# Kernel optimization log

Measured on AMD Instinct MI355X. Metric: run time of the kernel, lower is better.

Reference implementation:

```python
import jax, jax.numpy as jnp
import numpy as np

# Model dims (match init_kwargs)
D_OUT = 64      # d_in == d_out
SEQ_L = 4096    # input_len
K_EIG = 24      # num_eigh
K_U = 3         # auto_reg_k_u
K_Y = 2         # auto_reg_k_y
BATCH = 8


def get_top_hankel_eigh(n, k):
    """Top-k eigenpairs of the Hankel matrix Z[i,j] = 2/((i+j)^3-(i+j)), 1-indexed."""
    idx = np.arange(1, n + 1, dtype=np.float64)
    s = idx[:, None] + idx[None, :]
    z = 2.0 / (s ** 3 - s)
    vals, vecs = np.linalg.eigh(z)  # ascending
    return (jnp.asarray(vals[-k:], jnp.float32),        # [k]
            jnp.asarray(vecs[:, -k:], jnp.float32))     # [n, k]


def setup_inputs() -> dict:
    key = jax.random.key(0)
    k1, k2, k3, k4 = jax.random.split(key, 4)
    eig_vals, eig_vecs = get_top_hankel_eigh(SEQ_L, K_EIG)
    m_x_var = 1.0 / float(D_OUT) ** 0.5
    return {
        "inputs": jax.random.normal(k1, (BATCH, SEQ_L, D_OUT), jnp.float32),
        "m_y": jax.random.normal(k2, (D_OUT, K_Y, D_OUT), jnp.float32) * 0.01,
        "m_u": jax.random.normal(k3, (D_OUT, D_OUT, K_U), jnp.float32) * m_x_var,
        "m_phi": jax.random.normal(k4, (D_OUT * K_EIG, D_OUT), jnp.float32) * 0.01,
        "eig_vals": eig_vals,
        "eig_vecs": eig_vecs,
    }


def _stu_single(x, m_y, m_u, m_phi, eig_vals, eig_vecs):
    """apply_stu for one sequence x: [L, d] -> [L, d]."""
    L, d = x.shape
    n = 2 * L
    # --- compute_x_tilde: causal FFT conv of each eigenvector with each channel ---
    V = jnp.fft.rfft(eig_vecs, n=n, axis=0)             # [F, k]
    U = jnp.fft.rfft(x, n=n, axis=0)                    # [F, d]
    xt = jnp.fft.irfft(V[:, :, None] * U[:, None, :], n=n, axis=0)[:L]  # [L, k, d]
    xt = xt * (eig_vals ** 0.25)[None, :, None]
    x_tilde = xt.reshape(L, K_EIG * d)                  # [L, k*d]
    # --- delta_phi ---
    delta_phi = jnp.einsum('lk,kd->ld', x_tilde, m_phi)  # [L, d_out]
    # --- compute_ar_x_preds: shifted AR input contributions ---
    o = jnp.einsum('oik,li->klo', m_u, x)               # [k_u, L, d_out]
    shifts = jnp.arange(K_U)
    o = jax.vmap(lambda a, i: jnp.roll(a, i, axis=0))(o, shifts)
    mask = (jnp.arange(L)[None, :] >= shifts[:, None]).astype(x.dtype)  # [k_u, L]
    delta_ar_u = jnp.sum(o * mask[:, :, None], axis=0)  # [L, d_out]
    deltas = delta_phi + delta_ar_u
    # --- compute_y_t: sequential AR recurrence over time ---
    def step(carry, dlt):  # carry: [k_y, d_out]
        out = jnp.tensordot(m_y, carry, axes=2) + dlt    # [d_out]
        carry = jnp.roll(carry, 1, axis=0).at[0].set(out)
        return carry, out
    _, ys = jax.lax.scan(step, jnp.zeros((K_Y, d), x.dtype), deltas)
    return ys  # [L, d_out]


def reference(inputs, m_y, m_u, m_phi, eig_vals, eig_vecs):
    return jax.vmap(lambda x: _stu_single(x, m_y, m_u, m_phi, eig_vals, eig_vecs))(inputs)
```

## Files before the change

kernel.cpp:

```cpp
#include <hip/hip_runtime.h>
#include <math.h>

#define BB 8
#define LL 4096
#define DD 64
#define KK 24
#define KT 27
#define NN 8192
#define LOGN 13
#define NP 4128
#define NCH 256
#define CH 16

typedef unsigned int uint;
typedef unsigned short u16;
typedef __attribute__((ext_vector_type(8))) short bf16x8;
typedef __attribute__((ext_vector_type(4))) float f32x4;

__device__ __forceinline__ float bfl(uint u) {
    union { uint u; float f; } v; v.u = u << 16; return v.f;
}
__device__ __forceinline__ float bfh(uint u) {
    union { uint u; float f; } v; v.u = u & 0xFFFF0000u; return v.f;
}
__device__ __forceinline__ uint pk(float x) {
    union { float f; uint u; } v; v.f = x;
    return (v.u + 0x7FFFu + ((v.u >> 16) & 1u)) >> 16;
}
__device__ __forceinline__ float2 unpk2(uint u) {
    return make_float2(bfl(u), bfh(u));
}
__device__ __forceinline__ int br13(int v) { return (int)(__brev((uint)v) >> 19); }

template<int NT>
__device__ __forceinline__ void build_tw(float2* twc) {
    const int tid = threadIdx.x;
    for (int i = tid; i < 8192; i += NT) {
        if (i == 0) { twc[0] = make_float2(1.f, 0.f); continue; }
        int lh = 31 - __builtin_clz((uint)i);
        int j = i - (1 << lh);
        float ang = -6.28318530717958647692f * (float)j / (float)(2 << lh);
        float sn, cs;
        __sincosf(ang, &sn, &cs);
        twc[i] = make_float2(cs, sn);
    }
}

template<int NT>
__device__ __forceinline__ void fft_dif(float2* a, const float2* __restrict__ twc) {
    const int tid = threadIdx.x;
    for (int lh = LOGN - 1; lh >= 0; --lh) {
        const int half = 1 << lh;
#pragma unroll
        for (int bb = 0; bb < NN / 2 / NT; ++bb) {
            int t = tid + bb * NT;
            int j = t & (half - 1);
            int i0 = ((t >> lh) << (lh + 1)) + j;
            float2 u = a[i0], v = a[i0 + half];
            float2 w = twc[half + j];
            float cs = w.x, sn = w.y;
            float dx = u.x - v.x, dy = u.y - v.y;
            a[i0] = make_float2(u.x + v.x, u.y + v.y);
            a[i0 + half] = make_float2(dx * cs - dy * sn, dx * sn + dy * cs);
        }
        __syncthreads();
    }
}

template<int NT>
__device__ __forceinline__ void fft_dit(float2* a, const float2* __restrict__ twc) {
    const int tid = threadIdx.x;
    for (int lh = 0; lh < LOGN; ++lh) {
        const int half = 1 << lh;
#pragma unroll
        for (int bb = 0; bb < NN / 2 / NT; ++bb) {
            int t = tid + bb * NT;
            int j = t & (half - 1);
            int i0 = ((t >> lh) << (lh + 1)) + j;
            float2 u = a[i0], v = a[i0 + half];
            float2 w = twc[half + j];
            float cs = w.x, sn = -w.y;
            float wx = v.x * cs - v.y * sn;
            float wy = v.x * sn + v.y * cs;
            a[i0] = make_float2(u.x + wx, u.y + wy);
            a[i0 + half] = make_float2(u.x - wx, u.y - wy);
        }
        __syncthreads();
    }
}


__global__ __launch_bounds__(256) void k_pack(const float* __restrict__ mphi,
                                              const float* __restrict__ mu,
                                              uint* __restrict__ mp2) {
    int idx = blockIdx.x * 256 + threadIdx.x;
    if (idx >= KT * 2048) return;
    int k = idx >> 11;
    int rem = idx & 2047;
    int o = rem >> 5, cp = rem & 31;
    int c = cp * 2;
    uint v;
    if (k < KK) {
        v = pk(mphi[(k * 64 + c) * 64 + o]) | (pk(mphi[(k * 64 + c + 1) * 64 + o]) << 16);
    } else {
        int ku = k - KK;
        v = pk(mu[(o * 64 + c) * 3 + ku]) | (pk(mu[(o * 64 + c + 1) * 3 + ku]) << 16);
    }
    mp2[idx] = v;
}

__global__ __launch_bounds__(256) void k_fft_filters(const float* __restrict__ eig_vals,
                                                     const float* __restrict__ eig_vecs,
                                                     float2* __restrict__ Vb) {
    __shared__ float2 a[NN];
    __shared__ float2 twc[8192];
    const int k = blockIdx.x, tid = threadIdx.x;
    const float alpha = powf(eig_vals[k], 0.25f) * (1.0f / (float)NN);
    for (int t = tid; t < LL; t += 256)
        a[t] = make_float2(eig_vecs[t * KK + k] * alpha, 0.f);
    for (int t = LL + tid; t < NN; t += 256)
        a[t] = make_float2(0.f, 0.f);
    build_tw<256>(twc);
    __syncthreads();
    fft_dif<256>(a, twc);
    for (int r = tid; r < NN; r += 256)
        Vb[(size_t)r * KK + k] = a[r];
}

__global__ __launch_bounds__(512) void k_fft_x2(const float* __restrict__ x,
                                                uint* __restrict__ Uxp,
                                                uint* __restrict__ Uyp) {
    __shared__ float2 a[NN];
    __shared__ float2 twc[8192];
    const int b = blockIdx.x & 7, cp = blockIdx.x >> 3;
    const int tid = threadIdx.x;
    for (int l = tid; l < LL; l += 512)
        a[l] = *(const float2*)&x[((size_t)b * LL + l) * DD + 2 * cp];
    for (int l = LL + tid; l < NN; l += 512)
        a[l] = make_float2(0.f, 0.f);
    build_tw<512>(twc);
    __syncthreads();
    fft_dif<512>(a, twc);
    const size_t plane = ((size_t)b * 32 + cp) * NP;
    for (int idx = tid; idx < 4097; idx += 512) {
        int r = (idx == 4096) ? 1 : 2 * idx;
        int fn = br13(r);
        int q = br13((8192 - fn) & 8191);
        float2 Z = a[r], W = a[q];
        float ucx = 0.5f * (Z.x + W.x), ucy = 0.5f * (Z.y - W.y);
        float upx = 0.5f * (Z.y + W.y), upy = 0.5f * (W.x - Z.x);
        Uxp[plane + idx] = pk(ucx) | (pk(upx) << 16);
        Uyp[plane + idx] = pk(ucy) | (pk(upy) << 16);
    }
}

__global__ __launch_bounds__(256) void k_modulate5(const float2* __restrict__ Vb,
                                                   const uint* __restrict__ Uxp,
                                                   const uint* __restrict__ Uyp,
                                                   const uint* __restrict__ mp2,
                                                   uint* __restrict__ Sb2) {
    __shared__ u16 Uxs[32][72];
    __shared__ u16 Uys[32][72];
    __shared__ u16 mpT[2][64][72];
    __shared__ float2 Vt[32][28];
    const int tid = threadIdx.x;
    const int pt = blockIdx.x;
    const int b  = blockIdx.y;
    const int p0 = pt * 32;

    for (int i = tid; i < 1024; i += 256) {
        int cp = i >> 5, row = i & 31;
        uint vx = Uxp[((size_t)b * 32 + cp) * NP + p0 + row];
        uint vy = Uyp[((size_t)b * 32 + cp) * NP + p0 + row];
        *(uint*)&Uxs[row][cp * 2] = vx;
        *(uint*)&Uys[row][cp * 2] = vy;
    }
    {
        int o = tid >> 2, seg = tid & 3;
        const uint4* src = (const uint4*)&mp2[(size_t)o * 32 + seg * 8];
        uint4 m0 = src[0], m1 = src[1];
        *(uint4*)&mpT[0][o][seg * 16] = m0;
        *(uint4*)&mpT[0][o][seg * 16 + 8] = m1;
    }
    for (int i = tid; i < 768; i += 256) {
        int pi = i / 24, kk = i - pi * 24;
        int pidx = p0 + pi; if (pidx > 4096) pidx = 4096;
        int r = (pidx == 4096) ? 1 : 2 * pidx;
        Vt[pi][kk] = Vb[(size_t)r * KK + kk];
    }
    for (int pi = tid; pi < 32; pi += 256) {
        int pidx = p0 + pi; if (pidx > 4096) pidx = 4096;
        int r = (pidx == 4096) ? 1 : 2 * pidx;
        int f = br13(r);
        const float invN = 1.f / 8192.f;
        float ph = -6.28318530717958647692f * (float)f * invN;
        float s1, c1, s2, c2;
        __sincosf(ph, &s1, &c1);
        __sincosf(2.f * ph, &s2, &c2);
        Vt[pi][24] = make_float2(invN, 0.f);
        Vt[pi][25] = make_float2(c1 * invN, s1 * invN);
        Vt[pi][26] = make_float2(c2 * invN, s2 * invN);
    }
    __syncthreads();

    const int lane = tid & 63, w = tid >> 6;
    const int rt = w & 1, chalf = w >> 1;
    const int lrow = lane & 15, lk = lane >> 4;
    const u16* axp = &Uxs[rt * 16 + lrow][lk * 8];
    const u16* ayp = &Uys[rt * 16 + lrow][lk * 8];

    float Sx0[4] = {0.f, 0.f, 0.f, 0.f}, Sy0[4] = {0.f, 0.f, 0.f, 0.f};
    float Sx1[4] = {0.f, 0.f, 0.f, 0.f}, Sy1[4] = {0.f, 0.f, 0.f, 0.f};

    for (int k = 0; k < KT; ++k) {
        const int cur = k & 1;
        bf16x8 ax0 = *(const bf16x8*)(axp);
        bf16x8 ax1 = *(const bf16x8*)(axp + 32);
        bf16x8 ay0 = *(const bf16x8*)(ayp);
        bf16x8 ay1 = *(const bf16x8*)(ayp + 32);
        const u16* bp0 = &mpT[cur][chalf * 32 + lrow][lk * 8];
        const u16* bp1 = &mpT[cur][chalf * 32 + 16 + lrow][lk * 8];
        bf16x8 b00 = *(const bf16x8*)(bp0);
        bf16x8 b01 = *(const bf16x8*)(bp0 + 32);
        bf16x8 b10 = *(const bf16x8*)(bp1);
        bf16x8 b11 = *(const bf16x8*)(bp1 + 32);
        float2 v0 = Vt[rt * 16 + lk * 4 + 0][k];
        float2 v1 = Vt[rt * 16 + lk * 4 + 1][k];
        float2 v2 = Vt[rt * 16 + lk * 4 + 2][k];
        float2 v3 = Vt[rt * 16 + lk * 4 + 3][k];
        if (k + 1 < KT) {
            int o = tid >> 2, seg = tid & 3;
            const uint4* src = (const uint4*)&mp2[((size_t)(k + 1) * 64 + o) * 32 + seg * 8];
            uint4 m0 = src[0], m1 = src[1];
            *(uint4*)&mpT[cur ^ 1][o][seg * 16] = m0;
            *(uint4*)&mpT[cur ^ 1][o][seg * 16 + 8] = m1;
        }
        f32x4 z = {0.f, 0.f, 0.f, 0.f};
        f32x4 Wx0 = __builtin_amdgcn_mfma_f32_16x16x32_bf16(ax0, b00, z, 0, 0, 0);
        Wx0 = __builtin_amdgcn_mfma_f32_16x16x32_bf16(ax1, b01, Wx0, 0, 0, 0);
        f32x4 Wy0 = __builtin_amdgcn_mfma_f32_16x16x32_bf16(ay0, b00, z, 0, 0, 0);
        Wy0 = __builtin_amdgcn_mfma_f32_16x16x32_bf16(ay1, b01, Wy0, 0, 0, 0);
        f32x4 Wx1 = __builtin_amdgcn_mfma_f32_16x16x32_bf16(ax0, b10, z, 0, 0, 0);
        Wx1 = __builtin_amdgcn_mfma_f32_16x16x32_bf16(ax1, b11, Wx1, 0, 0, 0);
        f32x4 Wy1 = __builtin_amdgcn_mfma_f32_16x16x32_bf16(ay0, b10, z, 0, 0, 0);
        Wy1 = __builtin_amdgcn_mfma_f32_16x16x32_bf16(ay1, b11, Wy1, 0, 0, 0);
        Sx0[0] += v0.x * Wx0[0] - v0.y * Wy0[0];  Sy0[0] += v0.x * Wy0[0] + v0.y * Wx0[0];
        Sx0[1] += v1.x * Wx0[1] - v1.y * Wy0[1];  Sy0[1] += v1.x * Wy0[1] + v1.y * Wx0[1];
        Sx0[2] += v2.x * Wx0[2] - v2.y * Wy0[2];  Sy0[2] += v2.x * Wy0[2] + v2.y * Wx0[2];
        Sx0[3] += v3.x * Wx0[3] - v3.y * Wy0[3];  Sy0[3] += v3.x * Wy0[3] + v3.y * Wx0[3];
        Sx1[0] += v0.x * Wx1[0] - v0.y * Wy1[0];  Sy1[0] += v0.x * Wy1[0] + v0.y * Wx1[0];
        Sx1[1] += v1.x * Wx1[1] - v1.y * Wy1[1];  Sy1[1] += v1.x * Wy1[1] + v1.y * Wx1[1];
        Sx1[2] += v2.x * Wx1[2] - v2.y * Wy1[2];  Sy1[2] += v2.x * Wy1[2] + v2.y * Wx1[2];
        Sx1[3] += v3.x * Wx1[3] - v3.y * Wy1[3];  Sy1[3] += v3.x * Wy1[3] + v3.y * Wx1[3];
        __syncthreads();
    }
    const int rbase = rt * 16 + lk * 4;
    const int o0 = chalf * 32 + lrow;
    const size_t pl0 = ((size_t)b * 64 + o0) * NP + p0 + rbase;
    const size_t pl1 = ((size_t)b * 64 + o0 + 16) * NP + p0 + rbase;
#pragma unroll
    for (int j = 0; j < 4; ++j) {
        Sb2[pl0 + j] = pk(Sx0[j]) | (pk(Sy0[j]) << 16);
        Sb2[pl1 + j] = pk(Sx1[j]) | (pk(Sy1[j]) << 16);
    }
}

__global__ __launch_bounds__(512) void k_ifft2(const uint* __restrict__ Sb2,
                                               float* __restrict__ deltas) {
    __shared__ float2 a[NN];
    __shared__ float2 twc[8192];
    const int b = blockIdx.x & 7, op = blockIdx.x >> 3;
    const int tid = threadIdx.x;
    const uint* s0 = &Sb2[((size_t)b * 64 + op * 2) * NP];
    const uint* s1 = &Sb2[((size_t)b * 64 + op * 2 + 1) * NP];
    for (int idx = tid; idx < 4097; idx += 512) {
        int r = (idx == 4096) ? 1 : 2 * idx;
        float2 A = unpk2(s0[idx]), B = unpk2(s1[idx]);
        a[r] = make_float2(A.x - B.y, A.y + B.x);
        int fn = br13(r);
        int q = br13((8192 - fn) & 8191);
        if (q != r) a[q] = make_float2(A.x + B.y, B.x - A.y);
    }
    build_tw<512>(twc);
    __syncthreads();
    fft_dit<512>(a, twc);
    float* d0 = &deltas[((size_t)b * 64 + op * 2) * LL];
    float* d1 = &deltas[((size_t)b * 64 + op * 2 + 1) * LL];
    for (int l = tid; l < LL; l += 512) {
        d0[l] = a[l].x;
        d1[l] = a[l].y;
    }
}

__global__ __launch_bounds__(256) void k_matsq1(const float* __restrict__ m_y,
                                                float* __restrict__ C) {
    int idx = blockIdx.x * 256 + threadIdx.x;
    int r = idx >> 7, c = idx & 127;
    if (r >= 64) { C[idx] = m_y[(r - 64) * 128 + c]; return; }
    float acc = (c < 64) ? m_y[r * 128 + 64 + c] : 0.f;
#pragma unroll
    for (int i = 0; i < 64; ++i) acc += m_y[r * 128 + i] * m_y[i * 128 + c];
    C[idx] = acc;
}

__global__ __launch_bounds__(256) void k_matsq(const float* __restrict__ A,
                                               float* __restrict__ C) {
    int idx = blockIdx.x * 256 + threadIdx.x;
    int r = idx >> 7, c = idx & 127;
    float acc = 0.f;
#pragma unroll
    for (int i = 0; i < 128; ++i) acc += A[r * 128 + i] * A[i * 128 + c];
    C[idx] = acc;
}

__device__ __forceinline__ void load_rowhalf(const float* __restrict__ P, int r, int h,
                                             float* __restrict__ p) {
#pragma unroll
    for (int i4 = 0; i4 < 16; ++i4) {
        float4 v = *(const float4*)&P[r * 128 + h * 64 + i4 * 4];
        p[4 * i4] = v.x; p[4 * i4 + 1] = v.y; p[4 * i4 + 2] = v.z; p[4 * i4 + 3] = v.w;
    }
}
__device__ __forceinline__ float dot64(const float* __restrict__ p, const float* s) {
    float a0 = 0.f, a1 = 0.f, a2 = 0.f, a3 = 0.f;
#pragma unroll
    for (int i4 = 0; i4 < 16; ++i4) {
        float4 w = *(const float4*)&s[i4 * 4];
        a0 += p[4 * i4] * w.x;  a1 += p[4 * i4 + 1] * w.y;
        a2 += p[4 * i4 + 2] * w.z;  a3 += p[4 * i4 + 3] * w.w;
    }
    return (a0 + a1) + (a2 + a3);
}

__global__ __launch_bounds__(256, 1) void k_scan(const float* __restrict__ P,
                                                 const float* __restrict__ in,
                                                 float* __restrict__ partial,
                                                 float* __restrict__ terminal,
                                                 const int count) {
    const int bx = blockIdx.x;
    const int tid = threadIdx.x;
    const int r = tid & 127, h = tid >> 7;
    __shared__ __align__(16) float scur[128];
    __shared__ float pacc[256];
    float p[64];
    load_rowhalf(P, r, h, p);
    if (tid < 128) scur[tid] = 0.f;
    __syncthreads();
    const size_t base = (size_t)bx * count * 128;
    for (int k = 0; k < count; ++k) {
        if (tid < 128) partial[base + (size_t)k * 128 + tid] = scur[tid];
        pacc[tid] = dot64(p, &scur[h * 64]);
        __syncthreads();
        if (tid < 128) scur[tid] = pacc[tid] + pacc[tid + 128] + in[base + (size_t)k * 128 + tid];
        __syncthreads();
    }
    if (tid < 128) terminal[(size_t)bx * 128 + tid] = scur[tid];
}

__global__ __launch_bounds__(256, 1) void k_fixupg(const float* __restrict__ P,
                                                   const float* __restrict__ Sinit,
                                                   const float* __restrict__ q,
                                                   float* __restrict__ out,
                                                   const int count) {
    const int bx = blockIdx.x;
    const int tid = threadIdx.x;
    const int r = tid & 127, h = tid >> 7;
    __shared__ __align__(16) float scur[128];
    __shared__ float pacc[256];
    float p[64];
    load_rowhalf(P, r, h, p);
    if (tid < 128) scur[tid] = Sinit[(size_t)bx * 128 + tid];
    __syncthreads();
    const size_t base = (size_t)bx * count * 128;
    for (int k = 0; k < count; ++k) {
        if (tid < 128) out[base + (size_t)k * 128 + tid] = scur[tid] + q[base + (size_t)k * 128 + tid];
        if (k == count - 1) break;
        pacc[tid] = dot64(p, &scur[h * 64]);
        __syncthreads();
        if (tid < 128) scur[tid] = pacc[tid] + pacc[tid + 128];
        __syncthreads();
    }
}

__global__ __launch_bounds__(128, 1) void k_chunk_local(const float* __restrict__ deltas,
                                                        const float* __restrict__ m_y,
                                                        float* __restrict__ term) {
    const int b = blockIdx.x >> 8, j = blockIdx.x & 255;
    const int tid = threadIdx.x;
    const int o = tid & 63, h = tid >> 6;
    __shared__ __align__(16) float y1s[64];
    __shared__ __align__(16) float y2s[64];
    __shared__ float pacc[128];
    float m1[32], m2[32];
#pragma unroll
    for (int i4 = 0; i4 < 8; ++i4) {
        float4 v1 = *(const float4*)&m_y[o * 128 + h * 32 + i4 * 4];
        float4 v2 = *(const float4*)&m_y[o * 128 + 64 + h * 32 + i4 * 4];
        m1[4 * i4] = v1.x; m1[4 * i4 + 1] = v1.y; m1[4 * i4 + 2] = v1.z; m1[4 * i4 + 3] = v1.w;
        m2[4 * i4] = v2.x; m2[4 * i4 + 1] = v2.y; m2[4 * i4 + 2] = v2.z; m2[4 * i4 + 3] = v2.w;
    }
    if (tid < 64) { y1s[tid] = 0.f; y2s[tid] = 0.f; }
    __syncthreads();
    const float* dl = &deltas[((size_t)b * 64 + o) * LL + j * CH];
    for (int t = 0; t < CH; ++t) {
        float a0 = 0.f, a1 = 0.f, a2 = 0.f, a3 = 0.f;
#pragma unroll
        for (int i4 = 0; i4 < 8; ++i4) {
            float4 w1 = *(const float4*)&y1s[h * 32 + i4 * 4];
            float4 w2 = *(const float4*)&y2s[h * 32 + i4 * 4];
            a0 += m1[4 * i4] * w1.x + m2[4 * i4] * w2.x;
            a1 += m1[4 * i4 + 1] * w1.y + m2[4 * i4 + 1] * w2.y;
            a2 += m1[4 * i4 + 2] * w1.z + m2[4 * i4 + 2] * w2.z;
            a3 += m1[4 * i4 + 3] * w1.w + m2[4 * i4 + 3] * w2.w;
        }
        pacc[tid] = (a0 + a1) + (a2 + a3);
        __syncthreads();
        if (h == 0) {
            float outv = pacc[o] + pacc[o + 64] + dl[t];
            y2s[o] = y1s[o];
            y1s[o] = outv;
        }
        __syncthreads();
    }
    if (tid < 64) {
        term[((size_t)b * NCH + j) * 128 + o] = y1s[o];
        term[((size_t)b * NCH + j) * 128 + 64 + o] = y2s[o];
    }
}

__global__ __launch_bounds__(128, 1) void k_chunk_final(const float* __restrict__ deltas,
                                                        const float* __restrict__ m_y,
                                                        const float* __restrict__ sstate,
                                                        float* __restrict__ out) {
    const int b = blockIdx.x >> 8, j = blockIdx.x & 255;
    const int tid = threadIdx.x;
    const int o = tid & 63, h = tid >> 6;
    __shared__ __align__(16) float y1s[64];
    __shared__ __align__(16) float y2s[64];
    __shared__ float pacc[128];
    float m1[32], m2[32];
#pragma unroll
    for (int i4 = 0; i4 < 8; ++i4) {
        float4 v1 = *(const float4*)&m_y[o * 128 + h * 32 + i4 * 4];
        float4 v2 = *(const float4*)&m_y[o * 128 + 64 + h * 32 + i4 * 4];
        m1[4 * i4] = v1.x; m1[4 * i4 + 1] = v1.y; m1[4 * i4 + 2] = v1.z; m1[4 * i4 + 3] = v1.w;
        m2[4 * i4] = v2.x; m2[4 * i4 + 1] = v2.y; m2[4 * i4 + 2] = v2.z; m2[4 * i4 + 3] = v2.w;
    }
    if (tid < 64) {
        y1s[tid] = sstate[((size_t)b * NCH + j) * 128 + tid];
        y2s[tid] = sstate[((size_t)b * NCH + j) * 128 + 64 + tid];
    }
    __syncthreads();
    const float* dl = &deltas[((size_t)b * 64 + o) * LL + j * CH];
    const size_t obase = (((size_t)b * LL) + j * CH) * DD + o;
    for (int t = 0; t < CH; ++t) {
        float a0 = 0.f, a1 = 0.f, a2 = 0.f, a3 = 0.f;
#pragma unroll
        for (int i4 = 0; i4 < 8; ++i4) {
            float4 w1 = *(const float4*)&y1s[h * 32 + i4 * 4];
            float4 w2 = *(const float4*)&y2s[h * 32 + i4 * 4];
            a0 += m1[4 * i4] * w1.x + m2[4 * i4] * w2.x;
            a1 += m1[4 * i4 + 1] * w1.y + m2[4 * i4 + 1] * w2.y;
            a2 += m1[4 * i4 + 2] * w1.z + m2[4 * i4 + 2] * w2.z;
            a3 += m1[4 * i4 + 3] * w1.w + m2[4 * i4 + 3] * w2.w;
        }
        pacc[tid] = (a0 + a1) + (a2 + a3);
        __syncthreads();
        if (h == 0) {
            float outv = pacc[o] + pacc[o + 64] + dl[t];
            out[obase + (size_t)t * DD] = outv;
            y2s[o] = y1s[o];
            y1s[o] = outv;
        }
        __syncthreads();
    }
}

extern "C" void kernel_launch(void* const* d_in, const int* in_sizes, int n_in,
                              void* d_out, int out_size, void* d_ws, size_t ws_size,
                              hipStream_t stream) {
    const float* x        = (const float*)d_in[0];
    const float* m_y      = (const float*)d_in[1];
    const float* m_u      = (const float*)d_in[2];
    const float* m_phi    = (const float*)d_in[3];
    const float* eig_vals = (const float*)d_in[4];
    const float* eig_vecs = (const float*)d_in[5];
    float* out = (float*)d_out;

    char* ws = (char*)d_ws;
    size_t off = 0;
    auto alloc = [&](size_t bytes) -> void* {
        void* p = ws + off;
        off += (bytes + 255) & ~(size_t)255;
        return p;
    };
    float2* Vb   = (float2*)alloc((size_t)NN * KK * sizeof(float2));
    uint*   Uxp  = (uint*)alloc((size_t)BB * 32 * NP * sizeof(uint));
    uint*   Uyp  = (uint*)alloc((size_t)BB * 32 * NP * sizeof(uint));
    uint*   Sb2  = (uint*)alloc((size_t)BB * 64 * NP * sizeof(uint));
    float*  deltas = (float*)alloc((size_t)BB * 64 * LL * sizeof(float));
    uint*   mp2  = (uint*)alloc((size_t)KT * 64 * 32 * sizeof(uint));
    float*  mats = (float*)alloc((size_t)5 * 128 * 128 * sizeof(float));
    float*  term = (float*)alloc((size_t)BB * NCH * 128 * sizeof(float));
    float*  sst  = (float*)alloc((size_t)BB * NCH * 128 * sizeof(float));
    float*  qbuf = (float*)alloc((size_t)BB * NCH * 128 * sizeof(float));
    float*  Qg   = (float*)alloc((size_t)BB * 32 * 128 * sizeof(float));
    float*  q2   = (float*)alloc((size_t)BB * 32 * 128 * sizeof(float));
    float*  Sgt  = (float*)alloc((size_t)BB * 32 * 128 * sizeof(float));
    float*  Qsg  = (float*)alloc((size_t)BB * 4 * 128 * sizeof(float));
    float*  Ssg  = (float*)alloc((size_t)BB * 4 * 128 * sizeof(float));
    float*  dmy  = (float*)alloc((size_t)8 * 128 * sizeof(float));

    k_pack<<<dim3(216), dim3(256), 0, stream>>>(m_phi, m_u, mp2);
    k_fft_filters<<<dim3(24), dim3(256), 0, stream>>>(eig_vals, eig_vecs, Vb);
    k_fft_x2<<<dim3(256), dim3(512), 0, stream>>>(x, Uxp, Uyp);

    float* T1    = mats;
    float* T2    = mats + 16384;
    float* P16   = mats + 32768;
    float* P128  = mats + 49152;
    float* P1024 = mats + 65536;
    k_matsq1<<<dim3(64), dim3(256), 0, stream>>>(m_y, T1);
    k_matsq<<<dim3(64), dim3(256), 0, stream>>>(T1, T2);
    k_matsq<<<dim3(64), dim3(256), 0, stream>>>(T2, T1);
    k_matsq<<<dim3(64), dim3(256), 0, stream>>>(T1, P16);
    k_matsq<<<dim3(64), dim3(256), 0, stream>>>(P16, T1);
    k_matsq<<<dim3(64), dim3(256), 0, stream>>>(T1, T2);
    k_matsq<<<dim3(64), dim3(256), 0, stream>>>(T2, P128);
    k_matsq<<<dim3(64), dim3(256), 0, stream>>>(P128, T1);
    k_matsq<<<dim3(64), dim3(256), 0, stream>>>(T1, T2);
    k_matsq<<<dim3(64), dim3(256), 0, stream>>>(T2, P1024);

    k_modulate5<<<dim3(129, 8), dim3(256), 0, stream>>>(Vb, Uxp, Uyp, mp2, Sb2);
    k_ifft2<<<dim3(256), dim3(512), 0, stream>>>(Sb2, deltas);

    k_chunk_local<<<dim3(2048), dim3(128), 0, stream>>>(deltas, m_y, term);
    k_scan<<<dim3(256), dim3(256), 0, stream>>>(P16, term, qbuf, Qg, 8);
    k_scan<<<dim3(32), dim3(256), 0, stream>>>(P128, Qg, q2, Qsg, 8);
    k_scan<<<dim3(8), dim3(256), 0, stream>>>(P1024, Qsg, Ssg, dmy, 4);
    k_fixupg<<<dim3(32), dim3(256), 0, stream>>>(P128, Ssg, q2, Sgt, 8);
    k_fixupg<<<dim3(256), dim3(256), 0, stream>>>(P16, Sgt, qbuf, sst, 8);
    k_chunk_final<<<dim3(2048), dim3(128), 0, stream>>>(deltas, m_y, sst, out);
}
```

Baseline: 242.5 us.

## Enlarge modulate tile to 64 frequencies and triple-buffer weights via register prefetch

```diff
diff --git a/kernel.cpp b/kernel.cpp
--- a/kernel.cpp
+++ b/kernel.cpp
@@ -8,7 +8,7 @@
 #define KT 27
 #define NN 8192
 #define LOGN 13
-#define NP 4128
+#define NP 4160
 #define NCH 256
 #define CH 16
 
@@ -152,43 +152,40 @@
         Uxp[plane + idx] = pk(ucx) | (pk(upx) << 16);
         Uyp[plane + idx] = pk(ucy) | (pk(upy) << 16);
     }
-}
-
-__global__ __launch_bounds__(256) void k_modulate5(const float2* __restrict__ Vb,
+    for (int idx = 4097 + tid; idx < NP; idx += 512) {
+        Uxp[plane + idx] = 0;
+        Uyp[plane + idx] = 0;
+    }
+}
+
+__global__ __launch_bounds__(512) void k_modulate6(const float2* __restrict__ Vb,
                                                    const uint* __restrict__ Uxp,
                                                    const uint* __restrict__ Uyp,
                                                    const uint* __restrict__ mp2,
                                                    uint* __restrict__ Sb2) {
-    __shared__ u16 Uxs[32][72];
-    __shared__ u16 Uys[32][72];
-    __shared__ u16 mpT[2][64][72];
-    __shared__ float2 Vt[32][28];
-    const int tid = threadIdx.x;
-    const int pt = blockIdx.x;
+    __shared__ u16 Uxs[64][72];
+    __shared__ u16 Uys[64][72];
+    __shared__ u16 mpT[3][64][72];
+    __shared__ float2 Vt[64][28];
+    const int tid = threadIdx.x;
+    const int bx = blockIdx.x;
     const int b  = blockIdx.y;
-    const int p0 = pt * 32;
-
-    for (int i = tid; i < 1024; i += 256) {
-        int cp = i >> 5, row = i & 31;
+    const int p0 = bx * 64;
+
+    for (int i = tid; i < 2048; i += 512) {
+        int cp = i >> 6, row = i & 63;
         uint vx = Uxp[((size_t)b * 32 + cp) * NP + p0 + row];
         uint vy = Uyp[((size_t)b * 32 + cp) * NP + p0 + row];
         *(uint*)&Uxs[row][cp * 2] = vx;
         *(uint*)&Uys[row][cp * 2] = vy;
     }
-    {
-        int o = tid >> 2, seg = tid & 3;
-        const uint4* src = (const uint4*)&mp2[(size_t)o * 32 + seg * 8];
-        uint4 m0 = src[0], m1 = src[1];
-        *(uint4*)&mpT[0][o][seg * 16] = m0;
-        *(uint4*)&mpT[0][o][seg * 16 + 8] = m1;
-    }
-    for (int i = tid; i < 768; i += 256) {
+    for (int i = tid; i < 1536; i += 512) {
         int pi = i / 24, kk = i - pi * 24;
         int pidx = p0 + pi; if (pidx > 4096) pidx = 4096;
         int r = (pidx == 4096) ? 1 : 2 * pidx;
         Vt[pi][kk] = Vb[(size_t)r * KK + kk];
     }
-    for (int pi = tid; pi < 32; pi += 256) {
+    for (int pi = tid; pi < 64; pi += 512) {
         int pidx = p0 + pi; if (pidx > 4096) pidx = 4096;
         int r = (pidx == 4096) ? 1 : 2 * pidx;
         int f = br13(r);
@@ -201,10 +198,20 @@
         Vt[pi][25] = make_float2(c1 * invN, s1 * invN);
         Vt[pi][26] = make_float2(c2 * invN, s2 * invN);
     }
+    uint4 rA0, rA1;
+    const int so = tid >> 2, sseg = tid & 3;
+    if (tid < 256) {
+        const uint4* s0 = (const uint4*)&mp2[(size_t)so * 32 + sseg * 8];
+        uint4 m0 = s0[0], m1 = s0[1];
+        *(uint4*)&mpT[0][so][sseg * 16] = m0;
+        *(uint4*)&mpT[0][so][sseg * 16 + 8] = m1;
+        const uint4* s1 = (const uint4*)&mp2[(size_t)(64 + so) * 32 + sseg * 8];
+        rA0 = s1[0]; rA1 = s1[1];
+    }
     __syncthreads();
 
     const int lane = tid & 63, w = tid >> 6;
-    const int rt = w & 1, chalf = w >> 1;
+    const int rt = w & 3, chalf = w >> 2;
     const int lrow = lane & 15, lk = lane >> 4;
     const u16* axp = &Uxs[rt * 16 + lrow][lk * 8];
     const u16* ayp = &Uys[rt * 16 + lrow][lk * 8];
@@ -213,13 +220,23 @@
     float Sx1[4] = {0.f, 0.f, 0.f, 0.f}, Sy1[4] = {0.f, 0.f, 0.f, 0.f};
 
     for (int k = 0; k < KT; ++k) {
-        const int cur = k & 1;
+        uint4 rB0, rB1;
+        if (tid < 256 && k + 2 < KT) {
+            const uint4* src = (const uint4*)&mp2[((size_t)(k + 2) * 64 + so) * 32 + sseg * 8];
+            rB0 = src[0]; rB1 = src[1];
+        }
+        if (tid < 256 && k + 1 < KT) {
+            u16* dst = &mpT[(k + 1) % 3][so][sseg * 16];
+            *(uint4*)dst = rA0;
+            *(uint4*)(dst + 8) = rA1;
+        }
+        const u16* mb = &mpT[k % 3][0][0];
         bf16x8 ax0 = *(const bf16x8*)(axp);
         bf16x8 ax1 = *(const bf16x8*)(axp + 32);
         bf16x8 ay0 = *(const bf16x8*)(ayp);
         bf16x8 ay1 = *(const bf16x8*)(ayp + 32);
-        const u16* bp0 = &mpT[cur][chalf * 32 + lrow][lk * 8];
-        const u16* bp1 = &mpT[cur][chalf * 32 + 16 + lrow][lk * 8];
+        const u16* bp0 = mb + (chalf * 32 + lrow) * 72 + lk * 8;
+        const u16* bp1 = mb + (chalf * 32 + 16 + lrow) * 72 + lk * 8;
         bf16x8 b00 = *(const bf16x8*)(bp0);
         bf16x8 b01 = *(const bf16x8*)(bp0 + 32);
         bf16x8 b10 = *(const bf16x8*)(bp1);
@@ -228,13 +245,6 @@
         float2 v1 = Vt[rt * 16 + lk * 4 + 1][k];
         float2 v2 = Vt[rt * 16 + lk * 4 + 2][k];
         float2 v3 = Vt[rt * 16 + lk * 4 + 3][k];
-        if (k + 1 < KT) {
-            int o = tid >> 2, seg = tid & 3;
-            const uint4* src = (const uint4*)&mp2[((size_t)(k + 1) * 64 + o) * 32 + seg * 8];
-            uint4 m0 = src[0], m1 = src[1];
-            *(uint4*)&mpT[cur ^ 1][o][seg * 16] = m0;
-            *(uint4*)&mpT[cur ^ 1][o][seg * 16 + 8] = m1;
-        }
         f32x4 z = {0.f, 0.f, 0.f, 0.f};
         f32x4 Wx0 = __builtin_amdgcn_mfma_f32_16x16x32_bf16(ax0, b00, z, 0, 0, 0);
         Wx0 = __builtin_amdgcn_mfma_f32_16x16x32_bf16(ax1, b01, Wx0, 0, 0, 0);
@@ -252,6 +262,7 @@
         Sx1[1] += v1.x * Wx1[1] - v1.y * Wy1[1];  Sy1[1] += v1.x * Wy1[1] + v1.y * Wx1[1];
         Sx1[2] += v2.x * Wx1[2] - v2.y * Wy1[2];  Sy1[2] += v2.x * Wy1[2] + v2.y * Wx1[2];
         Sx1[3] += v3.x * Wx1[3] - v3.y * Wy1[3];  Sy1[3] += v3.x * Wy1[3] + v3.y * Wx1[3];
+        rA0 = rB0; rA1 = rB1;
         __syncthreads();
     }
     const int rbase = rt * 16 + lk * 4;
@@ -531,7 +542,7 @@
     k_matsq<<<dim3(64), dim3(256), 0, stream>>>(T1, T2);
     k_matsq<<<dim3(64), dim3(256), 0, stream>>>(T2, P1024);
 
-    k_modulate5<<<dim3(129, 8), dim3(256), 0, stream>>>(Vb, Uxp, Uyp, mp2, Sb2);
+    k_modulate6<<<dim3(65, 8), dim3(512), 0, stream>>>(Vb, Uxp, Uyp, mp2, Sb2);
     k_ifft2<<<dim3(256), dim3(512), 0, stream>>>(Sb2, deltas);
 
     k_chunk_local<<<dim3(2048), dim3(128), 0, stream>>>(deltas, m_y, term);
```

Result: slower. 586.7 us (+142.0%).
